# Kernel optimization log

Measured on AMD Instinct MI355X. Metric: run time of the kernel, lower is better.

Reference implementation:

```python
import jax, jax.numpy as jnp
import numpy as np

E, T, IN, OUT, S = 16, 16384, 1024, 4096, 256  # experts, total tokens, in_feat, out_feat, component rank


def setup_inputs() -> dict:
    key = jax.random.key(0)
    k0, k1, k2, k3 = jax.random.split(key, 4)
    inp = jax.random.normal(k0, (T, IN), jnp.float32)
    # tokens are pre-sorted by expert; equal load of T//E tokens per expert
    fwd_expert_count = jnp.full((E,), T // E, dtype=jnp.int32)
    # kaiming_uniform(a=sqrt(5)) on [out,in] ~ U(-1/sqrt(in), 1/sqrt(in))
    bw = 1.0 / np.sqrt(IN)
    weight = jax.random.uniform(k1, (E, OUT, IN), jnp.float32, -bw, bw)
    bias = jnp.zeros((E, OUT), jnp.float32)
    components = jax.random.normal(k2, (E, S, OUT), jnp.float32) * 0.02
    bu = 1.0 / np.sqrt(OUT)  # upscale_proj fan_in = source_dim = OUT
    upscale_proj = jax.random.uniform(k3, (E, S, OUT), jnp.float32, -bu, bu)
    upscale_bias = jnp.zeros((E, OUT), jnp.float32)
    return {
        "inp": inp,
        "fwd_expert_count": fwd_expert_count,
        "weight": weight,
        "bias": bias,
        "components": components,
        "upscale_proj": upscale_proj,
        "upscale_bias": upscale_bias,
    }


def reference(inp, fwd_expert_count, weight, bias, components, upscale_proj, upscale_bias):
    # fwd_expert_count is an int routing constant -> read concretely on host.
    counts = np.asarray(jax.device_get(fwd_expert_count))
    offsets = np.concatenate([np.zeros(1, np.int64), np.cumsum(counts)])
    n_exp = counts.shape[0]
    outs = []
    # Loop over the small, fixed expert set (grouped GEMM + per-expert projection).
    for e in range(n_exp):
        lo, hi = int(offsets[e]), int(offsets[e + 1])
        if hi == lo:
            continue
        seg = inp[lo:hi]                              # [c_e, IN]
        x = seg @ weight[e].T + bias[e]               # expert GEMM -> [c_e, OUT]
        p = x @ components[e].T                       # project onto components -> [c_e, S]
        y = p @ upscale_proj[e] + upscale_bias[e]     # upscale back -> [c_e, OUT]
        outs.append(y)
    return jnp.concatenate(outs, axis=0)              # [T, OUT]
```

## Files before the change

kernel.cpp:

```cpp
#include <hip/hip_runtime.h>
#include <hip/hip_bf16.h>

#define E_   16
#define T_   16384
#define IN_  1024
#define OUT_ 4096
#define S_   256
#define TPE  1024

typedef __attribute__((ext_vector_type(8))) short bf16x8;
typedef __attribute__((ext_vector_type(4))) float f32x4;

__device__ __forceinline__ unsigned short f2bf(float f) {
  union { float f; unsigned u; } x; x.f = f;
  unsigned r = x.u + 0x7fffu + ((x.u >> 16) & 1u);
  return (unsigned short)(r >> 16);
}

__global__ __launch_bounds__(256) void cvt_bf16(const float* __restrict__ src,
                                                unsigned short* __restrict__ dst) {
  size_t i = ((size_t)blockIdx.x * 256 + threadIdx.x) * 4;
  const float4 v = *(const float4*)(src + i);
  ushort4 o;
  o.x = f2bf(v.x); o.y = f2bf(v.y); o.z = f2bf(v.z); o.w = f2bf(v.w);
  *(ushort4*)(dst + i) = o;
}

__global__ __launch_bounds__(256) void transpose_cvt(const float* __restrict__ U,
                                                     unsigned short* __restrict__ Ut) {
  __shared__ float tile[32][33];
  const int e = blockIdx.z;
  const int o0 = blockIdx.x * 32, s0 = blockIdx.y * 32;
  const int tx = threadIdx.x, ty = threadIdx.y;
  const float* up = U + ((size_t)e * S_ + s0) * OUT_ + o0;
#pragma unroll
  for (int j = 0; j < 4; ++j)
    tile[ty + 8 * j][tx] = up[(size_t)(ty + 8 * j) * OUT_ + tx];
  __syncthreads();
  unsigned short* op = Ut + ((size_t)e * OUT_ + o0) * S_ + s0;
#pragma unroll
  for (int j = 0; j < 4; ++j)
    op[(size_t)(ty + 8 * j) * S_ + tx] = f2bf(tile[tx][ty + 8 * j]);
}

__device__ __forceinline__ void gld16(const unsigned short* g, unsigned short* l) {
  __builtin_amdgcn_global_load_lds(
      (const __attribute__((address_space(1))) void*)g,
      (__attribute__((address_space(3))) void*)l, 16, 0, 0);
}

template <int WMT, int WNT, typename OutT>
__global__ __launch_bounds__(256) void gemm_bt(
    const unsigned short* __restrict__ A, const unsigned short* __restrict__ Bt,
    OutT* __restrict__ C, const float* __restrict__ bias,
    int K, int lda, int ldb, int ldc,
    size_t sA, size_t sB, size_t sC, size_t sBias) {
  constexpr int BM = 32 * WMT;
  constexpr int BN = 32 * WNT;
  constexpr int BK = 32;
  __shared__ unsigned short lsA[BM * BK];
  __shared__ unsigned short lsB[BN * BK];

  const int t = threadIdx.x;
  const int wid = t >> 6, lane = t & 63;
  const int wr = wid >> 1, wc = wid & 1;
  const int fm = lane & 15, fk = (lane >> 4) * 8;

  const unsigned short* gA = A + blockIdx.z * sA + (size_t)(blockIdx.y * BM) * lda;
  const unsigned short* gB = Bt + blockIdx.z * sB + (size_t)(blockIdx.x * BN) * ldb;

  f32x4 acc[WMT][WNT];
#pragma unroll
  for (int i = 0; i < WMT; ++i)
#pragma unroll
    for (int j = 0; j < WNT; ++j) acc[i][j] = (f32x4){0.f, 0.f, 0.f, 0.f};

  for (int k0 = 0; k0 < K; k0 += BK) {
#pragma unroll
    for (int r = 0; r < BM / 64; ++r) {
      int idx = r * 256 + t;
      int row = idx >> 2;
      int kk = (idx & 3) * 8;
      gld16(gA + (size_t)row * lda + k0 + kk, &lsA[idx * 8]);
    }
#pragma unroll
    for (int r = 0; r < BN / 64; ++r) {
      int idx = r * 256 + t;
      int row = idx >> 2;
      int kk = (idx & 3) * 8;
      gld16(gB + (size_t)row * ldb + k0 + kk, &lsB[idx * 8]);
    }
    __syncthreads();

    bf16x8 afr[WMT], bfr[WNT];
#pragma unroll
    for (int i = 0; i < WMT; ++i)
      afr[i] = *(const bf16x8*)&lsA[(wr * 16 * WMT + i * 16 + fm) * BK + fk];
#pragma unroll
    for (int j = 0; j < WNT; ++j)
      bfr[j] = *(const bf16x8*)&lsB[(wc * 16 * WNT + j * 16 + fm) * BK + fk];
#pragma unroll
    for (int i = 0; i < WMT; ++i)
#pragma unroll
      for (int j = 0; j < WNT; ++j)
        acc[i][j] = __builtin_amdgcn_mfma_f32_16x16x32_bf16(afr[i], bfr[j], acc[i][j], 0, 0, 0);
    __syncthreads();
  }

  const int col = lane & 15;
  const int rbase = (lane >> 4) * 4;
  OutT* gC = C + blockIdx.z * sC;
  const float* gbias = bias ? bias + blockIdx.z * sBias : nullptr;
#pragma unroll
  for (int i = 0; i < WMT; ++i) {
    const int gm0 = blockIdx.y * BM + wr * 16 * WMT + i * 16 + rbase;
#pragma unroll
    for (int j = 0; j < WNT; ++j) {
      const int gn = blockIdx.x * BN + wc * 16 * WNT + j * 16 + col;
      const float bv = gbias ? gbias[gn] : 0.f;
#pragma unroll
      for (int r = 0; r < 4; ++r) {
        const float v = acc[i][j][r] + bv;
        const size_t off = (size_t)(gm0 + r) * ldc + gn;
        if constexpr (sizeof(OutT) == 2)
          ((unsigned short*)gC)[off] = f2bf(v);
        else
          ((float*)gC)[off] = v;
      }
    }
  }
}

extern "C" void kernel_launch(void* const* d_in, const int* in_sizes, int n_in,
                              void* d_out, int out_size, void* d_ws, size_t ws_size,
                              hipStream_t stream) {
  const float* inp    = (const float*)d_in[0];
  const float* weight = (const float*)d_in[2];
  const float* bias   = (const float*)d_in[3];
  const float* comps  = (const float*)d_in[4];
  const float* up     = (const float*)d_in[5];
  const float* upb    = (const float*)d_in[6];
  float* out = (float*)d_out;

  char* w = (char*)d_ws;
  unsigned short* A0 = (unsigned short*)w; w += (size_t)T_ * IN_ * 2;
  unsigned short* Wb = (unsigned short*)w; w += (size_t)E_ * OUT_ * IN_ * 2;
  unsigned short* Cb = (unsigned short*)w; w += (size_t)E_ * S_ * OUT_ * 2;
  unsigned short* Ub = (unsigned short*)w; w += (size_t)E_ * OUT_ * S_ * 2;
  unsigned short* X  = (unsigned short*)w; w += (size_t)T_ * OUT_ * 2;
  unsigned short* P  = (unsigned short*)w; w += (size_t)T_ * S_ * 2;

  cvt_bf16<<<(T_ * IN_) / 1024, 256, 0, stream>>>(inp, A0);
  cvt_bf16<<<(E_ * OUT_ * IN_) / 1024, 256, 0, stream>>>(weight, Wb);
  cvt_bf16<<<(E_ * S_ * OUT_) / 1024, 256, 0, stream>>>(comps, Cb);
  transpose_cvt<<<dim3(OUT_ / 32, S_ / 32, E_), dim3(32, 8), 0, stream>>>(up, Ub);

  gemm_bt<4, 4, unsigned short><<<dim3(OUT_ / 128, TPE / 128, E_), 256, 0, stream>>>(
      A0, Wb, X, bias, IN_, IN_, IN_, OUT_,
      (size_t)TPE * IN_, (size_t)OUT_ * IN_, (size_t)TPE * OUT_, (size_t)OUT_);

  gemm_bt<2, 4, unsigned short><<<dim3(S_ / 128, TPE / 64, E_), 256, 0, stream>>>(
      X, Cb, P, nullptr, OUT_, OUT_, OUT_, S_,
      (size_t)TPE * OUT_, (size_t)S_ * OUT_, (size_t)TPE * S_, 0);

  gemm_bt<4, 4, float><<<dim3(OUT_ / 128, TPE / 128, E_), 256, 0, stream>>>(
      P, Ub, out, upb, S_, S_, S_, OUT_,
      (size_t)TPE * S_, (size_t)OUT_ * S_, (size_t)TPE * OUT_, (size_t)OUT_);
}
```

Before: 998.1 us.

## Add 256x256 double-buffered swizzled GEMM for the expert and upscale GEMMs

```diff
diff --git a/kernel.cpp b/kernel.cpp
--- a/kernel.cpp
+++ b/kernel.cpp
@@ -47,6 +47,134 @@
   __builtin_amdgcn_global_load_lds(
       (const __attribute__((address_space(1))) void*)g,
       (__attribute__((address_space(3))) void*)l, 16, 0, 0);
+}
+
+template <typename OutT>
+__global__ __launch_bounds__(512, 2) void gemm_bt_8p(
+    const unsigned short* __restrict__ A, const unsigned short* __restrict__ Bt,
+    OutT* __restrict__ C, const float* __restrict__ bias,
+    int K, int lda, int ldb, int ldc,
+    size_t sA, size_t sB, size_t sC, size_t sBias) {
+  constexpr int BK = 64;
+  __shared__ unsigned short lsA[2][256 * BK];
+  __shared__ unsigned short lsB[2][256 * BK];
+
+  const int t = threadIdx.x;
+  const int lane = t & 63, wid = t >> 6;
+  const int wr = wid >> 1;
+  const int wc = wid & 1;
+  const int fm = lane & 15;
+  const int kq = lane >> 4;
+
+  const unsigned short* gA = A + blockIdx.z * sA + (size_t)(blockIdx.y * 256) * lda;
+  const unsigned short* gB = Bt + blockIdx.z * sB + (size_t)(blockIdx.x * 256) * ldb;
+
+  const int NT = K >> 6;
+
+  const int srow = t >> 3;
+  const int scp  = t & 7;
+
+  auto stage = [&](const unsigned short* g, int ldg, int k0, unsigned short* lds,
+                   int r0) {
+    const int row = r0 + srow;
+    const int cl = scp ^ (row & 7);
+    gld16(g + (size_t)row * ldg + k0 + cl * 8, lds + row * BK + scp * 8);
+  };
+  auto rdfrag = [&](const unsigned short* lds, int row, int kk) -> bf16x8 {
+    const int l = kk * 4 + kq;
+    return *(const bf16x8*)(lds + row * BK + ((l ^ (row & 7)) << 3));
+  };
+
+  f32x4 acc[4][8];
+#pragma unroll
+  for (int m = 0; m < 4; ++m)
+#pragma unroll
+    for (int n = 0; n < 8; ++n) acc[m][n] = (f32x4){0.f, 0.f, 0.f, 0.f};
+
+  stage(gA, lda, 0, lsA[0], 0);   stage(gA, lda, 0, lsA[0], 64);
+  stage(gA, lda, 0, lsA[0], 128); stage(gA, lda, 0, lsA[0], 192);
+  stage(gB, ldb, 0, lsB[0], 0);   stage(gB, ldb, 0, lsB[0], 128);
+  stage(gB, ldb, 0, lsB[0], 64);  stage(gB, ldb, 0, lsB[0], 192);
+  const int kp1 = (NT > 1 ? 1 : 0) << 6;
+  stage(gA, lda, kp1, lsA[1], 0);   stage(gA, lda, kp1, lsA[1], 64);
+  stage(gA, lda, kp1, lsA[1], 128); stage(gA, lda, kp1, lsA[1], 192);
+  stage(gB, ldb, kp1, lsB[1], 0);   stage(gB, ldb, kp1, lsB[1], 128);
+  asm volatile("s_waitcnt vmcnt(6)" ::: "memory");
+  __builtin_amdgcn_s_barrier();
+
+  int cur = 0;
+  for (int tau = 0; tau < NT; ++tau) {
+    const unsigned short* rA = lsA[cur];
+    const unsigned short* rB = lsB[cur];
+    unsigned short* nB1 = lsB[cur ^ 1];
+    unsigned short* nA2 = lsA[cur];
+    unsigned short* nB2 = lsB[cur];
+    const int k1 = (tau + 1 < NT ? tau + 1 : NT - 1) << 6;
+    const int k2 = (tau + 2 < NT ? tau + 2 : NT - 1) << 6;
+
+    bf16x8 af[4][2];
+    bf16x8 bf[2][2];
+#pragma unroll
+    for (int q = 0; q < 4; ++q) {
+      if (q == 0) {
+#pragma unroll
+        for (int m = 0; m < 4; ++m)
+#pragma unroll
+          for (int kk = 0; kk < 2; ++kk)
+            af[m][kk] = rdfrag(rA, wr * 64 + m * 16 + fm, kk);
+      }
+#pragma unroll
+      for (int j = 0; j < 2; ++j)
+#pragma unroll
+        for (int kk = 0; kk < 2; ++kk)
+          bf[j][kk] = rdfrag(rB, wc * 128 + (2 * q + j) * 16 + fm, kk);
+
+      if (q == 0)      { stage(gB, ldb, k1, nB1, 64);  stage(gB, ldb, k1, nB1, 192); }
+      else if (q == 1) { stage(gA, lda, k2, nA2, 0);   stage(gA, lda, k2, nA2, 64);  }
+      else if (q == 2) { stage(gA, lda, k2, nA2, 128); stage(gA, lda, k2, nA2, 192); }
+      else             { stage(gB, ldb, k2, nB2, 0);   stage(gB, ldb, k2, nB2, 128); }
+
+      __builtin_amdgcn_s_barrier();
+      asm volatile("s_waitcnt lgkmcnt(0)" ::: "memory");
+      __builtin_amdgcn_sched_barrier(0);
+      __builtin_amdgcn_s_setprio(1);
+#pragma unroll
+      for (int m = 0; m < 4; ++m)
+#pragma unroll
+        for (int j = 0; j < 2; ++j)
+#pragma unroll
+          for (int kk = 0; kk < 2; ++kk)
+            acc[m][2 * q + j] = __builtin_amdgcn_mfma_f32_16x16x32_bf16(
+                af[m][kk], bf[j][kk], acc[m][2 * q + j], 0, 0, 0);
+      __builtin_amdgcn_s_setprio(0);
+      if (q == 3) asm volatile("s_waitcnt vmcnt(6)" ::: "memory");
+      __builtin_amdgcn_s_barrier();
+    }
+    cur ^= 1;
+  }
+
+  const int col = lane & 15;
+  const int rb = kq * 4;
+  OutT* gC = C + blockIdx.z * sC;
+  const float* gbias = bias ? bias + blockIdx.z * sBias : nullptr;
+#pragma unroll
+  for (int m = 0; m < 4; ++m) {
+    const int gm0 = blockIdx.y * 256 + wr * 64 + m * 16 + rb;
+#pragma unroll
+    for (int n = 0; n < 8; ++n) {
+      const int gn = blockIdx.x * 256 + wc * 128 + n * 16 + col;
+      const float bv = gbias ? gbias[gn] : 0.f;
+#pragma unroll
+      for (int r = 0; r < 4; ++r) {
+        const float v = acc[m][n][r] + bv;
+        const size_t off = (size_t)(gm0 + r) * ldc + gn;
+        if constexpr (sizeof(OutT) == 2)
+          ((unsigned short*)gC)[off] = f2bf(v);
+        else
+          ((float*)gC)[off] = v;
+      }
+    }
+  }
 }
 
 template <int WMT, int WNT, typename OutT>
@@ -155,7 +283,7 @@
   cvt_bf16<<<(E_ * S_ * OUT_) / 1024, 256, 0, stream>>>(comps, Cb);
   transpose_cvt<<<dim3(OUT_ / 32, S_ / 32, E_), dim3(32, 8), 0, stream>>>(up, Ub);
 
-  gemm_bt<4, 4, unsigned short><<<dim3(OUT_ / 128, TPE / 128, E_), 256, 0, stream>>>(
+  gemm_bt_8p<unsigned short><<<dim3(OUT_ / 256, TPE / 256, E_), 512, 0, stream>>>(
       A0, Wb, X, bias, IN_, IN_, IN_, OUT_,
       (size_t)TPE * IN_, (size_t)OUT_ * IN_, (size_t)TPE * OUT_, (size_t)OUT_);
 
@@ -163,7 +291,7 @@
       X, Cb, P, nullptr, OUT_, OUT_, OUT_, S_,
       (size_t)TPE * OUT_, (size_t)S_ * OUT_, (size_t)TPE * S_, 0);
 
-  gemm_bt<4, 4, float><<<dim3(OUT_ / 128, TPE / 128, E_), 256, 0, stream>>>(
+  gemm_bt_8p<float><<<dim3(OUT_ / 256, TPE / 256, E_), 512, 0, stream>>>(
       P, Ub, out, upb, S_, S_, S_, OUT_,
       (size_t)TPE * S_, (size_t)OUT_ * S_, (size_t)TPE * OUT_, (size_t)OUT_);
 }
```

Result: faster. 947.7 us (-5.0%).
